# Optimization experiments

Hardware: AMD Instinct MI355X
Metric: run time of the kernel (lower is better)

Reference implementation:

```python
import jax, jax.numpy as jnp
import numpy as np

# Assumed sub-module definitions (NODETracker repo, sources not provided):
#   MLP(in,out)   = Linear -> LayerNorm -> LeakyReLU(0.1)
#   MLPODEF(dim,hidden,n_layers=2) = Linear(dim->h) -> tanh -> [Linear(h->h) -> tanh]*(n_layers-1) -> Linear(h->dim)
#   ode_solver_factory(None) -> fixed-step RK4, here 4 steps over t in [0,1]

LEAKY = 0.1
N_ODE_STEPS = 4
LATENT_DIM = 512
OBS_DIM = 256
HID_DIM = 1024
STATE = 2 * LATENT_DIM  # 1024
TIME_LEN = 128
BATCH = 512


def mlp_block(x, W, b, g, beta):
    h = x @ W + b
    mu = h.mean(-1, keepdims=True)
    var = ((h - mu) ** 2).mean(-1, keepdims=True)
    h = (h - mu) * jax.lax.rsqrt(var + 1e-5) * g + beta
    return jnp.where(h >= 0, h, LEAKY * h)


def odef(z, p):
    W0, b0, W1, b1, W2, b2 = p
    h = jnp.tanh(z @ W0 + b0)
    h = jnp.tanh(h @ W1 + b1)
    return h @ W2 + b2


def rk4_solve(z, p):
    dt = 1.0 / N_ODE_STEPS
    def step(z, _):
        k1 = odef(z, p)
        k2 = odef(z + 0.5 * dt * k1, p)
        k3 = odef(z + 0.5 * dt * k2, p)
        k4 = odef(z + dt * k3, p)
        return z + (dt / 6.0) * (k1 + 2 * k2 + 2 * k3 + k4), None
    z, _ = jax.lax.scan(step, z, None, length=N_ODE_STEPS)
    return z


def gru_step(x, h, W_ih, W_hh, b_ih, b_hh):
    gi = x @ W_ih.T + b_ih
    gh = h @ W_hh.T + b_hh
    i_r, i_z, i_n = jnp.split(gi, 3, axis=-1)
    h_r, h_z, h_n = jnp.split(gh, 3, axis=-1)
    r = jax.nn.sigmoid(i_r + h_r)
    zg = jax.nn.sigmoid(i_z + h_z)
    n = jnp.tanh(i_n + r * h_n)
    return (1.0 - zg) * n + zg * h


def setup_inputs() -> dict:
    key = jax.random.key(0)
    ks = jax.random.split(key, 16)
    def lin(k, fi, fo):
        return jax.random.normal(k, (fi, fo), jnp.float32) / np.sqrt(fi)
    return {
        'xs': jax.random.normal(ks[0], (TIME_LEN, BATCH, OBS_DIM), jnp.float32),
        'obs_W': lin(ks[1], OBS_DIM, HID_DIM), 'obs_b': jnp.zeros((HID_DIM,), jnp.float32),
        'obs_g': jnp.ones((HID_DIM,), jnp.float32), 'obs_beta': jnp.zeros((HID_DIM,), jnp.float32),
        'lat_W': lin(ks[2], HID_DIM, STATE), 'lat_b': jnp.zeros((STATE,), jnp.float32),
        'lat_g': jnp.ones((STATE,), jnp.float32), 'lat_beta': jnp.zeros((STATE,), jnp.float32),
        'ode_W0': lin(ks[3], STATE, HID_DIM), 'ode_b0': jnp.zeros((HID_DIM,), jnp.float32),
        'ode_W1': lin(ks[4], HID_DIM, HID_DIM), 'ode_b1': jnp.zeros((HID_DIM,), jnp.float32),
        'ode_W2': lin(ks[5], HID_DIM, STATE), 'ode_b2': jnp.zeros((STATE,), jnp.float32),
        'gru_Wih': jax.random.normal(ks[6], (3 * STATE, STATE), jnp.float32) / np.sqrt(STATE),
        'gru_Whh': jax.random.normal(ks[7], (3 * STATE, STATE), jnp.float32) / np.sqrt(STATE),
        'gru_bih': jnp.zeros((3 * STATE,), jnp.float32),
        'gru_bhh': jnp.zeros((3 * STATE,), jnp.float32),
    }


def reference(xs, obs_W, obs_b, obs_g, obs_beta, lat_W, lat_b, lat_g, lat_beta,
              ode_W0, ode_b0, ode_W1, ode_b1, ode_W2, ode_b2,
              gru_Wih, gru_Whh, gru_bih, gru_bhh):
    hs = mlp_block(xs, obs_W, obs_b, obs_g, obs_beta)          # [T,B,hid]
    zs = mlp_block(hs, lat_W, lat_b, lat_g, lat_beta)          # [T,B,2*latent]
    ode_p = (ode_W0, ode_b0, ode_W1, ode_b1, ode_W2, ode_b2)
    batch = xs.shape[1]
    h0 = jnp.zeros((batch, STATE), xs.dtype)

    def step(h, z_t):
        z = rk4_solve(z_t, ode_p)                               # NODE solve from t=0 to 1
        h_new = gru_step(z, h, gru_Wih, gru_Whh, gru_bih, gru_bhh)
        return h_new, None

    z0, _ = jax.lax.scan(step, h0, zs)                          # [B,2*latent]
    return z0[:, :LATENT_DIM], z0[:, LATENT_DIM:]
```

## Files before the change

### kernel.cpp

```cpp
#include <hip/hip_runtime.h>
#include <hip/hip_bf16.h>
#include <hip/hip_cooperative_groups.h>

namespace cg = cooperative_groups;

typedef __bf16 bf16_t;
typedef __bf16 bf16x8 __attribute__((ext_vector_type(8)));
typedef float f32x4 __attribute__((ext_vector_type(4)));

#define TLEN 128
#define BATCHN 512
#define OBS 256
#define HID 1024
#define STATEDIM 1024
#define ROWS (TLEN * BATCHN)
#define RKDT 0.25f

enum { EPI_F32 = 0, EPI_GI, EPI_TANH, EPI_Z0, EPI_Z0U, EPI_KW, EPI_KG, EPI_K4 };

__device__ __forceinline__ void gload_lds16(const bf16_t* g, bf16_t* l) {
  __builtin_amdgcn_global_load_lds(
      (const __attribute__((address_space(1))) void*)g,
      (__attribute__((address_space(3))) void*)l, 16, 0, 0);
}

__device__ __forceinline__ bf16_t f2bf(float x) { return (bf16_t)x; }

__device__ __forceinline__ float fast_tanh(float x) {
  const float e = __expf(2.f * x);
  return 1.f - 2.f / (e + 1.f);
}
__device__ __forceinline__ float fast_sigmoid(float x) {
  return 1.f / (1.f + __expf(-x));
}

#define MF(a_, b_, c_) __builtin_amdgcn_mfma_f32_16x16x32_bf16(a_, b_, c_, 0, 0, 0)

template<int EPI>
__global__ __launch_bounds__(256)
void gemm_bt(const bf16_t* __restrict__ A, const bf16_t* __restrict__ Wt,
             const float* __restrict__ bias, int M, int N, int K,
             float* outF, bf16_t* __restrict__ outB,
             float* Z, float* Z0,
             bf16_t* S2,
             const bf16_t* __restrict__ kb1, const bf16_t* __restrict__ kb2,
             const bf16_t* __restrict__ kb3,
             float kgc, int last)
{
  __shared__ __align__(16) bf16_t As[2][128 * 32];
  __shared__ __align__(16) bf16_t Bs[2][128 * 32];
  const int tid = threadIdx.x;
  const int lane = tid & 63;
  const int wave = tid >> 6;
  const int nbn = N >> 7;

  int bid = blockIdx.x;
  {
    const int nwg = gridDim.x;
    const int q = nwg >> 3, r = nwg & 7;
    const int xcd = bid & 7, lid = bid >> 3;
    bid = (xcd < r ? xcd * (q + 1) : r * (q + 1) + (xcd - r) * q) + lid;
  }
  const int bm = bid / nbn;
  const int bn = bid % nbn;
  const int m0 = bm << 7, n0 = bn << 7;
  const int wr = wave >> 1, wc = wave & 1;
  const int srow = tid >> 2;
  const int scol = (tid & 3) << 3;

  f32x4 acc[4][4] = {};
  const int nk = K >> 5;
  int cur = 0;

  {
    const bf16_t* ga = A  + (size_t)(m0 + srow) * K + scol;
    const bf16_t* gb = Wt + (size_t)(n0 + srow) * K + scol;
    bf16_t* la = &As[0][tid * 8];
    bf16_t* lb = &Bs[0][tid * 8];
    gload_lds16(ga, la);
    gload_lds16(ga + (size_t)64 * K, la + 2048);
    gload_lds16(gb, lb);
    gload_lds16(gb + (size_t)64 * K, lb + 2048);
  }

  for (int ks = 0; ks < nk; ++ks) {
    __syncthreads();
    if (ks + 1 < nk) {
      const bf16_t* ga = A  + (size_t)(m0 + srow) * K + (ks + 1) * 32 + scol;
      const bf16_t* gb = Wt + (size_t)(n0 + srow) * K + (ks + 1) * 32 + scol;
      bf16_t* la = &As[cur ^ 1][tid * 8];
      bf16_t* lb = &Bs[cur ^ 1][tid * 8];
      gload_lds16(ga, la);
      gload_lds16(ga + (size_t)64 * K, la + 2048);
      gload_lds16(gb, lb);
      gload_lds16(gb + (size_t)64 * K, lb + 2048);
    }
    const int kb = (lane >> 4) << 3;
    const int rr = lane & 15;
    bf16x8 af[4], bfr[4];
#pragma unroll
    for (int i = 0; i < 4; ++i) {
      af[i]  = *(const bf16x8*)&As[cur][(wr * 64 + i * 16 + rr) * 32 + kb];
      bfr[i] = *(const bf16x8*)&Bs[cur][(wc * 64 + i * 16 + rr) * 32 + kb];
    }
#pragma unroll
    for (int i = 0; i < 4; ++i)
#pragma unroll
      for (int j = 0; j < 4; ++j)
        acc[i][j] = MF(af[i], bfr[j], acc[i][j]);
    cur ^= 1;
  }

  const int cb = n0 + wc * 64 + (lane & 15);
  const int rb = m0 + wr * 64 + ((lane >> 4) << 2);
#pragma unroll
  for (int j = 0; j < 4; ++j) {
    const int c = cb + j * 16;
    float bv = 0.f;
    if constexpr (EPI != EPI_F32 && EPI != EPI_KG && EPI != EPI_Z0U) bv = bias[c];
#pragma unroll
    for (int i = 0; i < 4; ++i) {
      const int r0 = rb + i * 16;
#pragma unroll
      for (int r = 0; r < 4; ++r) {
        const size_t idx = (size_t)(r0 + r) * N + c;
        const float v = acc[i][j][r];
        if constexpr (EPI == EPI_F32) {
          outF[idx] = v;
        } else if constexpr (EPI == EPI_GI) {
          outF[idx] = v + bv;
        } else if constexpr (EPI == EPI_TANH) {
          outB[idx] = f2bf(fast_tanh(v + bv));
        } else if constexpr (EPI == EPI_Z0) {
          const float tz = v + bv;
          outF[idx] = tz;
          outB[idx] = f2bf(fast_tanh(tz));
        } else if constexpr (EPI == EPI_Z0U) {
          const float tz = Z0[idx] + v;
          Z0[idx] = tz;
          outB[idx] = f2bf(fast_tanh(tz));
        } else if constexpr (EPI == EPI_KW) {
          outB[idx] = f2bf(v + bv);
        } else if constexpr (EPI == EPI_KG) {
          outB[idx] = f2bf(fast_tanh(Z0[idx] + kgc * v));
        } else {
          const float k4 = v + bv;
          const float k1 = (float)kb1[idx];
          const float k2 = (float)kb2[idx];
          const float k3 = (float)kb3[idx];
          const float dz = (RKDT / 6.f) * (k1 + 2.f * k2 + 2.f * k3 + k4);
          const float zn = Z[idx] + dz;
          Z[idx] = zn;
          if (last) {
            const size_t si = (size_t)(r0 + r) * 2048 + c;
            const bf16_t hi = f2bf(zn);
            S2[si] = hi;
            S2[si + 1024] = f2bf(zn - (float)hi);
          } else {
            S2[idx] = f2bf(dz);
          }
        }
      }
    }
  }
}

__global__ __launch_bounds__(512)
void gru_persistent(const float* __restrict__ gi,
                    const bf16_t* __restrict__ Whh,
                    const float* __restrict__ bhh,
                    float* __restrict__ Hf,
                    bf16_t* __restrict__ hb,
                    unsigned int* __restrict__ ctr,
                    float* __restrict__ outp,
                    int TS, int t0)
{
  __shared__ __align__(16) bf16_t Bs[48 * 1032];
  const int tid  = threadIdx.x;
  const int lane = tid & 63;
  const int w    = tid >> 6;
  const int rg   = blockIdx.x >> 6;
  const int jg   = blockIdx.x & 63;
  const int r0   = rg << 7;
  const int j0   = jg << 4;

  for (int it = tid; it < 48 * 128; it += 512) {
    const int rr = it >> 7;
    const int co = (it & 127) << 3;
    const int g = rr >> 4, c = rr & 15;
    *(bf16x8*)&Bs[rr * 1032 + co] =
        *(const bf16x8*)&Whh[(size_t)(g * 1024 + j0 + c) * 1024 + co];
  }

  const int myj = j0 + (lane & 15);
  const float bh_r = bhh[myj], bh_z = bhh[1024 + myj], bh_n = bhh[2048 + myj];
  const int rbase = r0 + w * 16 + ((lane >> 4) << 2);

  float h[4];
#pragma unroll
  for (int q = 0; q < 4; ++q) h[q] = Hf[(size_t)(rbase + q) * 1024 + myj];

  float gpre[12];
  auto load_gi = [&](int lt) {
    const float* gir = gi + (size_t)lt * 512 * 3072;
#pragma unroll
    for (int q = 0; q < 4; ++q) {
      const size_t rr = (size_t)(rbase + q);
      gpre[q * 3 + 0] = gir[rr * 3072 + myj];
      gpre[q * 3 + 1] = gir[rr * 3072 + 1024 + myj];
      gpre[q * 3 + 2] = gir[rr * 3072 + 2048 + myj];
    }
  };
  load_gi(0);

  __syncthreads();

  const int arow = r0 + w * 16 + (lane & 15);
  const int akoff = (lane >> 4) << 3;

  for (int s = 0; s < TS; ++s) {
    const int t = t0 + s;
    const bf16_t* ap = hb + (size_t)(t & 1) * 512 * 2048 +
                       (size_t)arow * 2048 + akoff;
    f32x4 a0 = {}, a1 = {}, a2 = {};
    const bf16_t* bp0 = &Bs[(0  + (lane & 15)) * 1032 + akoff];
    const bf16_t* bp1 = &Bs[(16 + (lane & 15)) * 1032 + akoff];
    const bf16_t* bp2 = &Bs[(32 + (lane & 15)) * 1032 + akoff];
#pragma unroll 8
    for (int kc = 0; kc < 64; ++kc) {
      const bf16x8 af = *(const bf16x8*)(ap + kc * 32);
      const int kl = (kc * 32) & 1023;
      a0 = MF(af, *(const bf16x8*)(bp0 + kl), a0);
      a1 = MF(af, *(const bf16x8*)(bp1 + kl), a1);
      a2 = MF(af, *(const bf16x8*)(bp2 + kl), a2);
    }
    bf16_t* hbw = hb + (size_t)((t + 1) & 1) * 512 * 2048;
#pragma unroll
    for (int q = 0; q < 4; ++q) {
      const size_t rr = (size_t)(rbase + q);
      const float rg_ = fast_sigmoid(gpre[q * 3 + 0] + a0[q] + bh_r);
      const float zg  = fast_sigmoid(gpre[q * 3 + 1] + a1[q] + bh_z);
      const float n   = fast_tanh(gpre[q * 3 + 2] + rg_ * (a2[q] + bh_n));
      h[q] = (1.f - zg) * n + zg * h[q];
      union { __bf16 b; unsigned short u; } uh, ul;
      uh.b = f2bf(h[q]);
      ul.b = f2bf(h[q] - (float)uh.b);
      const unsigned ph = (unsigned)__shfl_xor((int)uh.u, 1) & 0xFFFFu;
      const unsigned pl = (unsigned)__shfl_xor((int)ul.u, 1) & 0xFFFFu;
      if (!(lane & 1)) {
        const unsigned hiw = (unsigned)uh.u | (ph << 16);
        const unsigned low = (unsigned)ul.u | (pl << 16);
        __hip_atomic_store((unsigned*)(hbw + rr * 2048 + myj), hiw,
                           __ATOMIC_RELAXED, __HIP_MEMORY_SCOPE_AGENT);
        __hip_atomic_store((unsigned*)(hbw + rr * 2048 + 1024 + myj), low,
                           __ATOMIC_RELAXED, __HIP_MEMORY_SCOPE_AGENT);
      }
    }
    if (s + 1 < TS) load_gi(s + 1);

    __syncthreads();
    if (tid == 0) {
      __hip_atomic_fetch_add(ctr, 1u, __ATOMIC_RELAXED, __HIP_MEMORY_SCOPE_AGENT);
      const unsigned tgt = 256u * (unsigned)(s + 1);
      while (__hip_atomic_load(ctr, __ATOMIC_ACQUIRE, __HIP_MEMORY_SCOPE_AGENT) < tgt)
        __builtin_amdgcn_s_sleep(1);
    }
    __syncthreads();
  }

#pragma unroll
  for (int q = 0; q < 4; ++q) {
    const int r = rbase + q;
    Hf[(size_t)r * 1024 + myj] = h[q];
    if (myj < 512) outp[(size_t)r * 512 + myj] = h[q];
    else           outp[262144 + (size_t)r * 512 + (myj - 512)] = h[q];
  }
}

__global__ void gru_reset(unsigned int* ctr) {
  if (threadIdx.x == 0)
    __hip_atomic_store(ctr, 0u, __ATOMIC_RELAXED, __HIP_MEMORY_SCOPE_AGENT);
}

template<bool SPLIT>
__global__ __launch_bounds__(256)
void ln_leaky(const float* __restrict__ pre, const float* __restrict__ b,
              const float* __restrict__ g, const float* __restrict__ bet,
              bf16_t* __restrict__ outB, float* __restrict__ zf)
{
  const int row = blockIdx.x;
  const int tid = threadIdx.x;
  const float* p = pre + (size_t)row * 1024;
  float v[4];
  float s = 0.f, s2 = 0.f;
#pragma unroll
  for (int i = 0; i < 4; ++i) {
    const int c = tid + i * 256;
    v[i] = p[c] + b[c];
    s += v[i]; s2 += v[i] * v[i];
  }
#pragma unroll
  for (int o = 32; o; o >>= 1) { s += __shfl_down(s, o); s2 += __shfl_down(s2, o); }
  __shared__ float rs[4], rs2[4];
  if ((tid & 63) == 0) { rs[tid >> 6] = s; rs2[tid >> 6] = s2; }
  __syncthreads();
  s = rs[0] + rs[1] + rs[2] + rs[3];
  s2 = rs2[0] + rs2[1] + rs2[2] + rs2[3];
  const float mu = s * (1.f / 1024.f);
  const float var = s2 * (1.f / 1024.f) - mu * mu;
  const float rstd = rsqrtf(var + 1e-5f);
#pragma unroll
  for (int i = 0; i < 4; ++i) {
    const int c = tid + i * 256;
    float h = (v[i] - mu) * rstd * g[c] + bet[c];
    h = h >= 0.f ? h : 0.1f * h;
    if constexpr (SPLIT) {
      const bf16_t hi = f2bf(h);
      outB[(size_t)row * 2048 + c] = hi;
      outB[(size_t)row * 2048 + 1024 + c] = f2bf(h - (float)hi);
      zf[(size_t)row * 1024 + c] = h;
    } else {
      outB[(size_t)row * 1024 + c] = f2bf(h);
    }
  }
}

__global__ __launch_bounds__(256)
void transpose_bf16(const float* __restrict__ in, bf16_t* __restrict__ out, int R, int C)
{
  __shared__ float t[32][33];
  const int c0 = blockIdx.x * 32, r0 = blockIdx.y * 32;
  const int tx = threadIdx.x & 31, ty = threadIdx.x >> 5;
#pragma unroll
  for (int i = 0; i < 32; i += 8)
    t[ty + i][tx] = in[(size_t)(r0 + ty + i) * C + c0 + tx];
  __syncthreads();
#pragma unroll
  for (int i = 0; i < 32; i += 8)
    out[(size_t)(c0 + ty + i) * R + r0 + tx] = f2bf(t[tx][ty + i]);
}

__global__ __launch_bounds__(256)
void f2b_kernel(const float* __restrict__ in, bf16_t* __restrict__ out, int n)
{
  const int i = blockIdx.x * 256 + threadIdx.x;
  if (i < n) out[i] = f2bf(in[i]);
}

__global__ __launch_bounds__(256)
void dup2_kernel(const bf16_t* __restrict__ in, bf16_t* __restrict__ out, int N, int K)
{
  const int idx = blockIdx.x * 256 + threadIdx.x;
  if (idx >= N * 2 * K) return;
  const int n = idx / (2 * K);
  const int kk = idx - n * 2 * K;
  const int k = kk < K ? kk : kk - K;
  out[idx] = in[(size_t)n * K + k];
}

__global__ void sentinel_kernel(float* out, float code) {
  if (threadIdx.x == 0 && blockIdx.x == 0) out[0] = code;
}

extern "C" void kernel_launch(void* const* d_in, const int* in_sizes, int n_in,
                              void* d_out, int out_size, void* d_ws, size_t ws_size,
                              hipStream_t stream)
{
  const float* xs    = (const float*)d_in[0];
  const float* obs_W = (const float*)d_in[1];
  const float* obs_b = (const float*)d_in[2];
  const float* obs_g = (const float*)d_in[3];
  const float* obs_be= (const float*)d_in[4];
  const float* lat_W = (const float*)d_in[5];
  const float* lat_b = (const float*)d_in[6];
  const float* lat_g = (const float*)d_in[7];
  const float* lat_be= (const float*)d_in[8];
  const float* W0    = (const float*)d_in[9];
  const float* b0    = (const float*)d_in[10];
  const float* W1    = (const float*)d_in[11];
  const float* b1    = (const float*)d_in[12];
  const float* W2    = (const float*)d_in[13];
  const float* b2    = (const float*)d_in[14];
  const float* Wih   = (const float*)d_in[15];
  const float* Whh   = (const float*)d_in[16];
  const float* bih   = (const float*)d_in[17];
  const float* bhh   = (const float*)d_in[18];

  char* ws = (char*)d_ws;
  size_t off = 0;
  auto alloc = [&](size_t bytes) { char* p = ws + off; off += bytes; return p; };

  bf16_t* OBSWT = (bf16_t*)alloc((size_t)HID * OBS * 2);
  bf16_t* LATWT = (bf16_t*)alloc((size_t)STATEDIM * HID * 2);
  bf16_t* W0T   = (bf16_t*)alloc((size_t)HID * STATEDIM * 2);
  bf16_t* W0T2  = (bf16_t*)alloc((size_t)HID * 2048 * 2);
  bf16_t* W1T   = (bf16_t*)alloc((size_t)HID * HID * 2);
  bf16_t* W2T   = (bf16_t*)alloc((size_t)STATEDIM * HID * 2);
  bf16_t* WIH2  = (bf16_t*)alloc((size_t)3072 * 2048 * 2);
  bf16_t* WHHB  = (bf16_t*)alloc((size_t)3072 * 1024 * 2);
  float*  Hf    = (float*)alloc((size_t)512 * 1024 * 4);
  bf16_t* HB2   = (bf16_t*)alloc((size_t)2 * 512 * 2048 * 2);
  bf16_t* WIHB  = (bf16_t*)alloc((size_t)3072 * 1024 * 2);
  bf16_t* XSB   = (bf16_t*)alloc((size_t)ROWS * OBS * 2);
  unsigned int* CTR = (unsigned int*)alloc(128);
  const size_t staticEnd = off;

  int nc = -1;
  const int ncs[8] = {1, 2, 4, 8, 16, 32, 64, 128};
  for (int i = 0; i < 8; ++i) {
    const size_t R = (size_t)ROWS / ncs[i];
    if (staticEnd + R * 22528 <= ws_size) { nc = ncs[i]; break; }
  }
  if (nc < 0) {
    sentinel_kernel<<<1, 1, 0, stream>>>((float*)d_out,
                                         -(1000000.0f + (float)(ws_size >> 20)));
    return;
  }
  const int R = ROWS / nc;
  char* arena = ws + staticEnd;
  float*  A1f  = (float*)(arena);
  bf16_t* KB1  = (bf16_t*)(arena);
  bf16_t* KB2  = (bf16_t*)(arena + (size_t)R * 2048);
  float*  Zf   = (float*)(arena + (size_t)R * 4096);
  float*  Z0f  = (float*)(arena + (size_t)R * 8192);
  bf16_t* H1b  = (bf16_t*)(arena + (size_t)R * 12288);
  bf16_t* H2b  = (bf16_t*)(arena + (size_t)R * 14336);
  bf16_t* KB3  = (bf16_t*)(arena + (size_t)R * 16384);
  bf16_t* S2b  = (bf16_t*)(arena + (size_t)R * 18432);
  bf16_t* DZb  = S2b;
  float*  GIf  = (float*)(arena);

  auto gemm = [&](int epi, const bf16_t* A, const bf16_t* Wt, const float* bias,
                  int M, int N, int K, float* oF, bf16_t* oB,
                  float kgc = 0.f, int last = 0) {
    dim3 g((M / 128) * (N / 128)), b(256);
    switch (epi) {
      case EPI_F32:  gemm_bt<EPI_F32><<<g, b, 0, stream>>>(A, Wt, bias, M, N, K, oF, oB, Zf, Z0f, S2b, KB1, KB2, KB3, kgc, last); break;
      case EPI_GI:   gemm_bt<EPI_GI><<<g, b, 0, stream>>>(A, Wt, bias, M, N, K, oF, oB, Zf, Z0f, S2b, KB1, KB2, KB3, kgc, last); break;
      case EPI_TANH: gemm_bt<EPI_TANH><<<g, b, 0, stream>>>(A, Wt, bias, M, N, K, oF, oB, Zf, Z0f, S2b, KB1, KB2, KB3, kgc, last); break;
      case EPI_Z0:   gemm_bt<EPI_Z0><<<g, b, 0, stream>>>(A, Wt, bias, M, N, K, oF, oB, Zf, Z0f, S2b, KB1, KB2, KB3, kgc, last); break;
      case EPI_Z0U:  gemm_bt<EPI_Z0U><<<g, b, 0, stream>>>(A, Wt, bias, M, N, K, oF, oB, Zf, Z0f, S2b, KB1, KB2, KB3, kgc, last); break;
      case EPI_KW:   gemm_bt<EPI_KW><<<g, b, 0, stream>>>(A, Wt, bias, M, N, K, oF, oB, Zf, Z0f, S2b, KB1, KB2, KB3, kgc, last); break;
      case EPI_KG:   gemm_bt<EPI_KG><<<g, b, 0, stream>>>(A, Wt, bias, M, N, K, oF, oB, Zf, Z0f, S2b, KB1, KB2, KB3, kgc, last); break;
      case EPI_K4:   gemm_bt<EPI_K4><<<g, b, 0, stream>>>(A, Wt, bias, M, N, K, oF, oB, Zf, Z0f, S2b, KB1, KB2, KB3, kgc, last); break;
    }
  };

  transpose_bf16<<<dim3(HID / 32, OBS / 32), 256, 0, stream>>>(obs_W, OBSWT, OBS, HID);
  transpose_bf16<<<dim3(STATEDIM / 32, HID / 32), 256, 0, stream>>>(lat_W, LATWT, HID, STATEDIM);
  transpose_bf16<<<dim3(HID / 32, STATEDIM / 32), 256, 0, stream>>>(W0, W0T, STATEDIM, HID);
  dup2_kernel<<<(HID * 2048) / 256, 256, 0, stream>>>(W0T, W0T2, HID, 1024);
  transpose_bf16<<<dim3(HID / 32, HID / 32), 256, 0, stream>>>(W1, W1T, HID, HID);
  transpose_bf16<<<dim3(STATEDIM / 32, HID / 32), 256, 0, stream>>>(W2, W2T, HID, STATEDIM);
  f2b_kernel<<<(3072 * 1024) / 256, 256, 0, stream>>>(Wih, WIHB, 3072 * 1024);
  dup2_kernel<<<(3072 * 2048) / 256, 256, 0, stream>>>(WIHB, WIH2, 3072, 1024);
  f2b_kernel<<<(3072 * 1024) / 256, 256, 0, stream>>>(Whh, WHHB, 3072 * 1024);
  f2b_kernel<<<(ROWS * OBS) / 256, 256, 0, stream>>>(xs, XSB, ROWS * OBS);

  hipMemsetAsync(Hf, 0, (size_t)512 * 1024 * 4, stream);
  hipMemsetAsync(HB2, 0, (size_t)2 * 512 * 2048 * 2, stream);
  const int TS = R / BATCHN;

  for (int c = 0; c < nc; ++c) {
    gemm(EPI_F32, XSB + (size_t)c * R * OBS, OBSWT, nullptr, R, HID, OBS, A1f, nullptr);
    ln_leaky<false><<<R, 256, 0, stream>>>(A1f, obs_b, obs_g, obs_be, H1b, nullptr);
    gemm(EPI_F32, H1b, LATWT, nullptr, R, STATEDIM, HID, A1f, nullptr);
    ln_leaky<true><<<R, 256, 0, stream>>>(A1f, lat_b, lat_g, lat_be, S2b, Zf);

    for (int step = 0; step < 4; ++step) {
      if (step == 0) gemm(EPI_Z0, S2b, W0T2, b0, R, HID, 2048, Z0f, H1b);
      else           gemm(EPI_Z0U, DZb, W0T, nullptr, R, HID, 1024, nullptr, H1b);
      gemm(EPI_TANH, H1b, W1T, b1, R, HID, HID, nullptr, H2b);
      gemm(EPI_KW, H2b, W2T, b2, R, STATEDIM, HID, nullptr, KB1);
      gemm(EPI_KG, KB1, W0T, nullptr, R, HID, STATEDIM, nullptr, H1b, 0.5f * RKDT);
      gemm(EPI_TANH, H1b, W1T, b1, R, HID, HID, nullptr, H2b);
      gemm(EPI_KW, H2b, W2T, b2, R, STATEDIM, HID, nullptr, KB2);
      gemm(EPI_KG, KB2, W0T, nullptr, R, HID, STATEDIM, nullptr, H1b, 0.5f * RKDT);
      gemm(EPI_TANH, H1b, W1T, b1, R, HID, HID, nullptr, H2b);
      gemm(EPI_KW, H2b, W2T, b2, R, STATEDIM, HID, nullptr, KB3);
      gemm(EPI_KG, KB3, W0T, nullptr, R, HID, STATEDIM, nullptr, H1b, RKDT);
      gemm(EPI_TANH, H1b, W1T, b1, R, HID, HID, nullptr, H2b);
      gemm(EPI_K4, H2b, W2T, b2, R, STATEDIM, HID, nullptr, nullptr, 0.f,
           (step == 3) ? 1 : 0);
    }

    gemm(EPI_GI, S2b, WIH2, bih, R, 3072, 2048, GIf, nullptr);

    gru_reset<<<1, 64, 0, stream>>>(CTR);
    {
      const float* giArg = GIf;
      const bf16_t* whhArg = WHHB;
      const float* bhhArg = bhh;
      float* hfArg = Hf;
      bf16_t* hbArg = HB2;
      unsigned int* ctrArg = CTR;
      float* outArg = (float*)d_out;
      int tsArg = TS;
      int t0Arg = c * TS;
      void* args[] = { (void*)&giArg, (void*)&whhArg, (void*)&bhhArg,
                       (void*)&hfArg, (void*)&hbArg, (void*)&ctrArg,
                       (void*)&outArg, (void*)&tsArg, (void*)&t0Arg };
      hipLaunchCooperativeKernel((const void*)gru_persistent,
                                 dim3(256), dim3(512), args, 0, stream);
    }
  }
}
```

Measured before the change: 18.83 ms.

## Fuse RK4 ODE GEMM chain into one cooperative persistent kernel with grid barriers

Runs the 52 per-chunk ODE GEMM stages inside a single cooperatively launched persistent kernel. Blocks loop over 128x128 tiles in an XCD-aware order and synchronise between stages with an atomic-counter grid barrier. Epilogue stores become agent-scope relaxed atomic stores, packed as bf16 pairs through lane shuffles, so writes are visible across the grid. This is meant to remove per-launch overhead and inter-kernel gaps, at the cost of barrier spin time, occupancy capped at two blocks per CU, and the extra shuffle work on the store path. The original multi-launch path stays as a fallback if the cooperative launch fails.

```diff
diff --git a/kernel.cpp b/kernel.cpp
--- a/kernel.cpp
+++ b/kernel.cpp
@@ -75,12 +75,10 @@
   {
     const bf16_t* ga = A  + (size_t)(m0 + srow) * K + scol;
     const bf16_t* gb = Wt + (size_t)(n0 + srow) * K + scol;
-    bf16_t* la = &As[0][tid * 8];
-    bf16_t* lb = &Bs[0][tid * 8];
-    gload_lds16(ga, la);
-    gload_lds16(ga + (size_t)64 * K, la + 2048);
-    gload_lds16(gb, lb);
-    gload_lds16(gb + (size_t)64 * K, lb + 2048);
+    gload_lds16(ga, &As[0][tid * 8]);
+    gload_lds16(ga + (size_t)64 * K, &As[0][tid * 8] + 2048);
+    gload_lds16(gb, &Bs[0][tid * 8]);
+    gload_lds16(gb + (size_t)64 * K, &Bs[0][tid * 8] + 2048);
   }
 
   for (int ks = 0; ks < nk; ++ks) {
@@ -88,12 +86,10 @@
     if (ks + 1 < nk) {
       const bf16_t* ga = A  + (size_t)(m0 + srow) * K + (ks + 1) * 32 + scol;
       const bf16_t* gb = Wt + (size_t)(n0 + srow) * K + (ks + 1) * 32 + scol;
-      bf16_t* la = &As[cur ^ 1][tid * 8];
-      bf16_t* lb = &Bs[cur ^ 1][tid * 8];
-      gload_lds16(ga, la);
-      gload_lds16(ga + (size_t)64 * K, la + 2048);
-      gload_lds16(gb, lb);
-      gload_lds16(gb + (size_t)64 * K, lb + 2048);
+      gload_lds16(ga, &As[cur ^ 1][tid * 8]);
+      gload_lds16(ga + (size_t)64 * K, &As[cur ^ 1][tid * 8] + 2048);
+      gload_lds16(gb, &Bs[cur ^ 1][tid * 8]);
+      gload_lds16(gb + (size_t)64 * K, &Bs[cur ^ 1][tid * 8] + 2048);
     }
     const int kb = (lane >> 4) << 3;
     const int rr = lane & 15;
@@ -165,6 +161,197 @@
   }
 }
 
+__device__ __forceinline__ void sc1_f32(float* p, float v) {
+  __hip_atomic_store(p, v, __ATOMIC_RELAXED, __HIP_MEMORY_SCOPE_AGENT);
+}
+__device__ __forceinline__ void sc1_bf16pair(bf16_t* base, size_t idx, float val, int lane) {
+  union { __bf16 b; unsigned short u; } t; t.b = f2bf(val);
+  const unsigned other = (unsigned)__shfl_xor((int)t.u, 1) & 0xFFFFu;
+  if (!(lane & 1)) {
+    const unsigned wv = (unsigned)t.u | (other << 16);
+    __hip_atomic_store((unsigned*)(base + idx), wv,
+                       __ATOMIC_RELAXED, __HIP_MEMORY_SCOPE_AGENT);
+  }
+}
+
+__device__ __forceinline__ void grid_bar(unsigned* ctr, int bar) {
+  __syncthreads();
+  if (threadIdx.x == 0) {
+    __hip_atomic_fetch_add(ctr, 1u, __ATOMIC_RELAXED, __HIP_MEMORY_SCOPE_AGENT);
+    const unsigned tgt = (unsigned)gridDim.x * (unsigned)bar;
+    while (__hip_atomic_load(ctr, __ATOMIC_ACQUIRE, __HIP_MEMORY_SCOPE_AGENT) < tgt)
+      __builtin_amdgcn_s_sleep(1);
+  }
+  __syncthreads();
+}
+
+template<int EPI>
+__device__ void ode_stage(const bf16_t* __restrict__ A, const bf16_t* __restrict__ Wt,
+                          const float* __restrict__ bias, int R, int K,
+                          float kgc, int last,
+                          float* Zf, float* Z0f, bf16_t* outB, bf16_t* S2,
+                          const bf16_t* __restrict__ kb1, const bf16_t* __restrict__ kb2,
+                          const bf16_t* __restrict__ kb3,
+                          bf16_t* as_base, bf16_t* bs_base)
+{
+  const int tid = threadIdx.x;
+  const int lane = tid & 63;
+  const int wave = tid >> 6;
+  const int wr = wave >> 1, wc = wave & 1;
+  const int srow = tid >> 2;
+  const int scol = (tid & 3) << 3;
+  const int nk = K >> 5;
+  const int ntiles = (R >> 7) << 3;
+  const int cpx = ntiles >> 3;
+
+  for (int tt = blockIdx.x; tt < ntiles; tt += gridDim.x) {
+    const int ts = (tt & 7) * cpx + (tt >> 3);
+    const int m0 = (ts >> 3) << 7, n0 = (ts & 7) << 7;
+    f32x4 acc[4][4] = {};
+    int cur = 0;
+    {
+      const bf16_t* ga = A  + (size_t)(m0 + srow) * K + scol;
+      const bf16_t* gb = Wt + (size_t)(n0 + srow) * K + scol;
+      gload_lds16(ga, as_base + tid * 8);
+      gload_lds16(ga + (size_t)64 * K, as_base + tid * 8 + 2048);
+      gload_lds16(gb, bs_base + tid * 8);
+      gload_lds16(gb + (size_t)64 * K, bs_base + tid * 8 + 2048);
+    }
+    for (int ks = 0; ks < nk; ++ks) {
+      __syncthreads();
+      if (ks + 1 < nk) {
+        const bf16_t* ga = A  + (size_t)(m0 + srow) * K + (ks + 1) * 32 + scol;
+        const bf16_t* gb = Wt + (size_t)(n0 + srow) * K + (ks + 1) * 32 + scol;
+        gload_lds16(ga, as_base + (cur ^ 1) * 4096 + tid * 8);
+        gload_lds16(ga + (size_t)64 * K, as_base + (cur ^ 1) * 4096 + tid * 8 + 2048);
+        gload_lds16(gb, bs_base + (cur ^ 1) * 4096 + tid * 8);
+        gload_lds16(gb + (size_t)64 * K, bs_base + (cur ^ 1) * 4096 + tid * 8 + 2048);
+      }
+      const int kb = (lane >> 4) << 3;
+      const int rr = lane & 15;
+      bf16x8 af[4], bfr[4];
+#pragma unroll
+      for (int i = 0; i < 4; ++i) {
+        af[i]  = *(const bf16x8*)(as_base + cur * 4096 + (wr * 64 + i * 16 + rr) * 32 + kb);
+        bfr[i] = *(const bf16x8*)(bs_base + cur * 4096 + (wc * 64 + i * 16 + rr) * 32 + kb);
+      }
+#pragma unroll
+      for (int i = 0; i < 4; ++i)
+#pragma unroll
+        for (int j = 0; j < 4; ++j)
+          acc[i][j] = MF(af[i], bfr[j], acc[i][j]);
+      cur ^= 1;
+    }
+
+    const int cb = n0 + wc * 64 + (lane & 15);
+    const int rb = m0 + wr * 64 + ((lane >> 4) << 2);
+#pragma unroll
+    for (int j = 0; j < 4; ++j) {
+      const int c = cb + j * 16;
+      float bv = 0.f;
+      if constexpr (EPI == EPI_Z0 || EPI == EPI_TANH || EPI == EPI_KW || EPI == EPI_K4)
+        bv = bias[c];
+#pragma unroll
+      for (int i = 0; i < 4; ++i) {
+        const int r0 = rb + i * 16;
+#pragma unroll
+        for (int r = 0; r < 4; ++r) {
+          const size_t idx = (size_t)(r0 + r) * 1024 + c;
+          const float v = acc[i][j][r];
+          if constexpr (EPI == EPI_Z0) {
+            const float tz = v + bv;
+            sc1_f32(&Z0f[idx], tz);
+            sc1_bf16pair(outB, idx, fast_tanh(tz), lane);
+          } else if constexpr (EPI == EPI_Z0U) {
+            const float tz = Z0f[idx] + v;
+            sc1_f32(&Z0f[idx], tz);
+            sc1_bf16pair(outB, idx, fast_tanh(tz), lane);
+          } else if constexpr (EPI == EPI_TANH) {
+            sc1_bf16pair(outB, idx, fast_tanh(v + bv), lane);
+          } else if constexpr (EPI == EPI_KW) {
+            sc1_bf16pair(outB, idx, v + bv, lane);
+          } else if constexpr (EPI == EPI_KG) {
+            sc1_bf16pair(outB, idx, fast_tanh(Z0f[idx] + kgc * v), lane);
+          } else {
+            const float k4 = v + bv;
+            const float k1 = (float)kb1[idx];
+            const float k2 = (float)kb2[idx];
+            const float k3 = (float)kb3[idx];
+            const float dz = (RKDT / 6.f) * (k1 + 2.f * k2 + 2.f * k3 + k4);
+            const float zn = Zf[idx] + dz;
+            sc1_f32(&Zf[idx], zn);
+            if (last) {
+              const size_t si = (size_t)(r0 + r) * 2048 + c;
+              const float hi = (float)f2bf(zn);
+              sc1_bf16pair(S2, si, zn, lane);
+              sc1_bf16pair(S2, si + 1024, zn - hi, lane);
+            } else {
+              sc1_bf16pair(S2, idx, dz, lane);
+            }
+          }
+        }
+      }
+    }
+  }
+}
+
+__global__ __launch_bounds__(256, 2)
+void ode_persistent(const bf16_t* __restrict__ W0T2, const bf16_t* __restrict__ W0T,
+                    const bf16_t* __restrict__ W1T, const bf16_t* __restrict__ W2T,
+                    const float* __restrict__ b0, const float* __restrict__ b1,
+                    const float* __restrict__ b2,
+                    float* Zf, float* Z0f, bf16_t* H1b, bf16_t* H2b,
+                    bf16_t* KB1, bf16_t* KB2, bf16_t* KB3, bf16_t* S2b,
+                    unsigned* ctr, int R)
+{
+  __shared__ __align__(16) bf16_t As[2 * 4096];
+  __shared__ __align__(16) bf16_t Bs[2 * 4096];
+  int bar = 0;
+#pragma unroll 1
+  for (int step = 0; step < 4; ++step) {
+    if (step == 0)
+      ode_stage<EPI_Z0>(S2b, W0T2, b0, R, 2048, 0.f, 0, Zf, Z0f, H1b, S2b,
+                        nullptr, nullptr, nullptr, As, Bs);
+    else
+      ode_stage<EPI_Z0U>(S2b, W0T, nullptr, R, 1024, 0.f, 0, Zf, Z0f, H1b, S2b,
+                         nullptr, nullptr, nullptr, As, Bs);
+    grid_bar(ctr, ++bar);
+    ode_stage<EPI_TANH>(H1b, W1T, b1, R, 1024, 0.f, 0, Zf, Z0f, H2b, S2b,
+                        nullptr, nullptr, nullptr, As, Bs);
+    grid_bar(ctr, ++bar);
+    ode_stage<EPI_KW>(H2b, W2T, b2, R, 1024, 0.f, 0, Zf, Z0f, KB1, S2b,
+                      nullptr, nullptr, nullptr, As, Bs);
+    grid_bar(ctr, ++bar);
+    ode_stage<EPI_KG>(KB1, W0T, nullptr, R, 1024, 0.5f * RKDT, 0, Zf, Z0f, H1b, S2b,
+                      nullptr, nullptr, nullptr, As, Bs);
+    grid_bar(ctr, ++bar);
+    ode_stage<EPI_TANH>(H1b, W1T, b1, R, 1024, 0.f, 0, Zf, Z0f, H2b, S2b,
+                        nullptr, nullptr, nullptr, As, Bs);
+    grid_bar(ctr, ++bar);
+    ode_stage<EPI_KW>(H2b, W2T, b2, R, 1024, 0.f, 0, Zf, Z0f, KB2, S2b,
+                      nullptr, nullptr, nullptr, As, Bs);
+    grid_bar(ctr, ++bar);
+    ode_stage<EPI_KG>(KB2, W0T, nullptr, R, 1024, 0.5f * RKDT, 0, Zf, Z0f, H1b, S2b,
+                      nullptr, nullptr, nullptr, As, Bs);
+    grid_bar(ctr, ++bar);
+    ode_stage<EPI_TANH>(H1b, W1T, b1, R, 1024, 0.f, 0, Zf, Z0f, H2b, S2b,
+                        nullptr, nullptr, nullptr, As, Bs);
+    grid_bar(ctr, ++bar);
+    ode_stage<EPI_KW>(H2b, W2T, b2, R, 1024, 0.f, 0, Zf, Z0f, KB3, S2b,
+                      nullptr, nullptr, nullptr, As, Bs);
+    grid_bar(ctr, ++bar);
+    ode_stage<EPI_KG>(KB3, W0T, nullptr, R, 1024, RKDT, 0, Zf, Z0f, H1b, S2b,
+                      nullptr, nullptr, nullptr, As, Bs);
+    grid_bar(ctr, ++bar);
+    ode_stage<EPI_TANH>(H1b, W1T, b1, R, 1024, 0.f, 0, Zf, Z0f, H2b, S2b,
+                        nullptr, nullptr, nullptr, As, Bs);
+    grid_bar(ctr, ++bar);
+    ode_stage<EPI_K4>(H2b, W2T, b2, R, 1024, 0.f, (step == 3) ? 1 : 0,
+                      Zf, Z0f, nullptr, S2b, KB1, KB2, KB3, As, Bs);
+    grid_bar(ctr, ++bar);
+  }
+}
+
 __global__ __launch_bounds__(512)
 void gru_persistent(const float* __restrict__ gi,
                     const bf16_t* __restrict__ Whh,
@@ -277,7 +464,7 @@
   }
 }
 
-__global__ void gru_reset(unsigned int* ctr) {
+__global__ void ctr_reset(unsigned int* ctr) {
   if (threadIdx.x == 0)
     __hip_atomic_store(ctr, 0u, __ATOMIC_RELAXED, __HIP_MEMORY_SCOPE_AGENT);
 }
@@ -402,7 +589,8 @@
   bf16_t* HB2   = (bf16_t*)alloc((size_t)2 * 512 * 2048 * 2);
   bf16_t* WIHB  = (bf16_t*)alloc((size_t)3072 * 1024 * 2);
   bf16_t* XSB   = (bf16_t*)alloc((size_t)ROWS * OBS * 2);
-  unsigned int* CTR = (unsigned int*)alloc(128);
+  unsigned int* GCTR = (unsigned int*)alloc(128);
+  unsigned int* OCTR = (unsigned int*)alloc(128);
   const size_t staticEnd = off;
 
   int nc = -1;
@@ -461,39 +649,64 @@
   hipMemsetAsync(HB2, 0, (size_t)2 * 512 * 2048 * 2, stream);
   const int TS = R / BATCHN;
 
+  int occ = 0;
+  (void)hipOccupancyMaxActiveBlocksPerMultiprocessor(
+      &occ, (const void*)ode_persistent, 256, 0);
+  const int odeBlocks = (occ >= 2) ? 512 : (occ == 1 ? 256 : 0);
+
   for (int c = 0; c < nc; ++c) {
     gemm(EPI_F32, XSB + (size_t)c * R * OBS, OBSWT, nullptr, R, HID, OBS, A1f, nullptr);
     ln_leaky<false><<<R, 256, 0, stream>>>(A1f, obs_b, obs_g, obs_be, H1b, nullptr);
     gemm(EPI_F32, H1b, LATWT, nullptr, R, STATEDIM, HID, A1f, nullptr);
     ln_leaky<true><<<R, 256, 0, stream>>>(A1f, lat_b, lat_g, lat_be, S2b, Zf);
 
-    for (int step = 0; step < 4; ++step) {
-      if (step == 0) gemm(EPI_Z0, S2b, W0T2, b0, R, HID, 2048, Z0f, H1b);
-      else           gemm(EPI_Z0U, DZb, W0T, nullptr, R, HID, 1024, nullptr, H1b);
-      gemm(EPI_TANH, H1b, W1T, b1, R, HID, HID, nullptr, H2b);
-      gemm(EPI_KW, H2b, W2T, b2, R, STATEDIM, HID, nullptr, KB1);
-      gemm(EPI_KG, KB1, W0T, nullptr, R, HID, STATEDIM, nullptr, H1b, 0.5f * RKDT);
-      gemm(EPI_TANH, H1b, W1T, b1, R, HID, HID, nullptr, H2b);
-      gemm(EPI_KW, H2b, W2T, b2, R, STATEDIM, HID, nullptr, KB2);
-      gemm(EPI_KG, KB2, W0T, nullptr, R, HID, STATEDIM, nullptr, H1b, 0.5f * RKDT);
-      gemm(EPI_TANH, H1b, W1T, b1, R, HID, HID, nullptr, H2b);
-      gemm(EPI_KW, H2b, W2T, b2, R, STATEDIM, HID, nullptr, KB3);
-      gemm(EPI_KG, KB3, W0T, nullptr, R, HID, STATEDIM, nullptr, H1b, RKDT);
-      gemm(EPI_TANH, H1b, W1T, b1, R, HID, HID, nullptr, H2b);
-      gemm(EPI_K4, H2b, W2T, b2, R, STATEDIM, HID, nullptr, nullptr, 0.f,
-           (step == 3) ? 1 : 0);
+    bool persisted = false;
+    if (odeBlocks > 0) {
+      ctr_reset<<<1, 64, 0, stream>>>(OCTR);
+      const bf16_t* a0_ = W0T2; const bf16_t* a1_ = W0T;
+      const bf16_t* a2_ = W1T;  const bf16_t* a3_ = W2T;
+      const float* a4_ = b0; const float* a5_ = b1; const float* a6_ = b2;
+      float* a7_ = Zf; float* a8_ = Z0f;
+      bf16_t* a9_ = H1b; bf16_t* a10_ = H2b;
+      bf16_t* a11_ = KB1; bf16_t* a12_ = KB2; bf16_t* a13_ = KB3;
+      bf16_t* a14_ = S2b;
+      unsigned int* a15_ = OCTR; int a16_ = R;
+      void* args[] = { &a0_, &a1_, &a2_, &a3_, &a4_, &a5_, &a6_, &a7_, &a8_,
+                       &a9_, &a10_, &a11_, &a12_, &a13_, &a14_, &a15_, &a16_ };
+      hipError_t e = hipLaunchCooperativeKernel((const void*)ode_persistent,
+                                                dim3(odeBlocks), dim3(256),
+                                                args, 0, stream);
+      persisted = (e == hipSuccess);
+    }
+    if (!persisted) {
+      for (int step = 0; step < 4; ++step) {
+        if (step == 0) gemm(EPI_Z0, S2b, W0T2, b0, R, HID, 2048, Z0f, H1b);
+        else           gemm(EPI_Z0U, DZb, W0T, nullptr, R, HID, 1024, nullptr, H1b);
+        gemm(EPI_TANH, H1b, W1T, b1, R, HID, HID, nullptr, H2b);
+        gemm(EPI_KW, H2b, W2T, b2, R, STATEDIM, HID, nullptr, KB1);
+        gemm(EPI_KG, KB1, W0T, nullptr, R, HID, STATEDIM, nullptr, H1b, 0.5f * RKDT);
+        gemm(EPI_TANH, H1b, W1T, b1, R, HID, HID, nullptr, H2b);
+        gemm(EPI_KW, H2b, W2T, b2, R, STATEDIM, HID, nullptr, KB2);
+        gemm(EPI_KG, KB2, W0T, nullptr, R, HID, STATEDIM, nullptr, H1b, 0.5f * RKDT);
+        gemm(EPI_TANH, H1b, W1T, b1, R, HID, HID, nullptr, H2b);
+        gemm(EPI_KW, H2b, W2T, b2, R, STATEDIM, HID, nullptr, KB3);
+        gemm(EPI_KG, KB3, W0T, nullptr, R, HID, STATEDIM, nullptr, H1b, RKDT);
+        gemm(EPI_TANH, H1b, W1T, b1, R, HID, HID, nullptr, H2b);
+        gemm(EPI_K4, H2b, W2T, b2, R, STATEDIM, HID, nullptr, nullptr, 0.f,
+             (step == 3) ? 1 : 0);
+      }
     }
 
     gemm(EPI_GI, S2b, WIH2, bih, R, 3072, 2048, GIf, nullptr);
 
-    gru_reset<<<1, 64, 0, stream>>>(CTR);
+    ctr_reset<<<1, 64, 0, stream>>>(GCTR);
     {
       const float* giArg = GIf;
       const bf16_t* whhArg = WHHB;
       const float* bhhArg = bhh;
       float* hfArg = Hf;
       bf16_t* hbArg = HB2;
-      unsigned int* ctrArg = CTR;
+      unsigned int* ctrArg = GCTR;
       float* outArg = (float*)d_out;
       int tsArg = TS;
       int t0Arg = c * TS;
```

After: 31.96 ms. 1.7x slower.

## Fold W0 into W2 to fuse RK stage GEMMs and accumulate stages in fp32

Applied to the files above, without the earlier changes.

Precomputes the combined weight W0·W2 and bias, and concatenates it with W2 so each RK stage runs one N=2048 GEMM. That GEMM produces both k and the next stage's pre-activation directly, instead of a W2 GEMM followed by a W0 GEMM on k. Stage contributions are accumulated in fp32 KACC/GACC buffers, and Z0 is updated in the fourth-stage epilogue, which removes the per-step Z0 update GEMM and the bf16 k buffers. This reduces launches and intermediate memory traffic, at the cost of wider epilogue branches and slightly different numerics from the pre-multiplied weights.

```diff
diff --git a/kernel.cpp b/kernel.cpp
--- a/kernel.cpp
+++ b/kernel.cpp
@@ -16,7 +16,7 @@
 #define ROWS (TLEN * BATCHN)
 #define RKDT 0.25f
 
-enum { EPI_F32 = 0, EPI_GI, EPI_TANH, EPI_Z0, EPI_Z0U, EPI_KW, EPI_KG, EPI_K4 };
+enum { EPI_F32 = 0, EPI_GI, EPI_TANH, EPI_B16, EPI_Z0, EPI_F1, EPI_F23, EPI_F4, EPI_K4L };
 
 __device__ __forceinline__ void gload_lds16(const bf16_t* g, bf16_t* l) {
   __builtin_amdgcn_global_load_lds(
@@ -41,10 +41,8 @@
 void gemm_bt(const bf16_t* __restrict__ A, const bf16_t* __restrict__ Wt,
              const float* __restrict__ bias, int M, int N, int K,
              float* outF, bf16_t* __restrict__ outB,
-             float* Z, float* Z0,
-             bf16_t* S2,
-             const bf16_t* __restrict__ kb1, const bf16_t* __restrict__ kb2,
-             const bf16_t* __restrict__ kb3,
+             float* Z, float* Z0, bf16_t* S2,
+             float* KACC, float* GACC,
              float kgc, int last)
 {
   __shared__ __align__(16) bf16_t As[2][128 * 32];
@@ -117,7 +115,7 @@
   for (int j = 0; j < 4; ++j) {
     const int c = cb + j * 16;
     float bv = 0.f;
-    if constexpr (EPI != EPI_F32 && EPI != EPI_KG && EPI != EPI_Z0U) bv = bias[c];
+    if constexpr (EPI != EPI_F32 && EPI != EPI_B16) bv = bias[c];
 #pragma unroll
     for (int i = 0; i < 4; ++i) {
       const int r0 = rb + i * 16;
@@ -131,34 +129,45 @@
           outF[idx] = v + bv;
         } else if constexpr (EPI == EPI_TANH) {
           outB[idx] = f2bf(fast_tanh(v + bv));
+        } else if constexpr (EPI == EPI_B16) {
+          outB[idx] = f2bf(v);
         } else if constexpr (EPI == EPI_Z0) {
           const float tz = v + bv;
           outF[idx] = tz;
           outB[idx] = f2bf(fast_tanh(tz));
-        } else if constexpr (EPI == EPI_Z0U) {
-          const float tz = Z0[idx] + v;
-          Z0[idx] = tz;
-          outB[idx] = f2bf(fast_tanh(tz));
-        } else if constexpr (EPI == EPI_KW) {
-          outB[idx] = f2bf(v + bv);
-        } else if constexpr (EPI == EPI_KG) {
-          outB[idx] = f2bf(fast_tanh(Z0[idx] + kgc * v));
+        } else if constexpr (EPI == EPI_F1 || EPI == EPI_F23) {
+          if (c < 1024) {
+            const size_t ix = (size_t)(r0 + r) * 1024 + c;
+            const float kv = v + bv;
+            if constexpr (EPI == EPI_F1) KACC[ix] = (RKDT / 6.f) * kv;
+            else                         KACC[ix] += (RKDT / 3.f) * kv;
+          } else {
+            const size_t ix = (size_t)(r0 + r) * 1024 + (c - 1024);
+            const float Gv = v + bv;
+            outB[ix] = f2bf(fast_tanh(Z0[ix] + kgc * Gv));
+            if constexpr (EPI == EPI_F1) GACC[ix] = (RKDT / 6.f) * Gv;
+            else                         GACC[ix] += (RKDT / 3.f) * Gv;
+          }
+        } else if constexpr (EPI == EPI_F4) {
+          if (c < 1024) {
+            const size_t ix = (size_t)(r0 + r) * 1024 + c;
+            const float kv = v + bv;
+            Z[ix] = Z[ix] + KACC[ix] + (RKDT / 6.f) * kv;
+          } else {
+            const size_t ix = (size_t)(r0 + r) * 1024 + (c - 1024);
+            const float Gv = v + bv;
+            const float z0n = Z0[ix] + GACC[ix] + (RKDT / 6.f) * Gv;
+            Z0[ix] = z0n;
+            outB[ix] = f2bf(fast_tanh(z0n));
+          }
         } else {
-          const float k4 = v + bv;
-          const float k1 = (float)kb1[idx];
-          const float k2 = (float)kb2[idx];
-          const float k3 = (float)kb3[idx];
-          const float dz = (RKDT / 6.f) * (k1 + 2.f * k2 + 2.f * k3 + k4);
-          const float zn = Z[idx] + dz;
+          const float kv = v + bv;
+          const float zn = Z[idx] + KACC[idx] + (RKDT / 6.f) * kv;
           Z[idx] = zn;
-          if (last) {
-            const size_t si = (size_t)(r0 + r) * 2048 + c;
-            const bf16_t hi = f2bf(zn);
-            S2[si] = hi;
-            S2[si + 1024] = f2bf(zn - (float)hi);
-          } else {
-            S2[idx] = f2bf(dz);
-          }
+          const size_t si = (size_t)(r0 + r) * 2048 + c;
+          const bf16_t hi = f2bf(zn);
+          S2[si] = hi;
+          S2[si + 1024] = f2bf(zn - (float)hi);
         }
       }
     }
@@ -358,6 +367,18 @@
   out[idx] = in[(size_t)n * K + k];
 }
 
+__global__ __launch_bounds__(256)
+void biaskg_kernel(const float* __restrict__ b2, const float* __restrict__ W0,
+                   float* __restrict__ biasKG)
+{
+  const int n = blockIdx.x * 256 + threadIdx.x;
+  if (n >= 1024) return;
+  biasKG[n] = b2[n];
+  float s = 0.f;
+  for (int ss = 0; ss < 1024; ++ss) s += b2[ss] * W0[(size_t)ss * 1024 + n];
+  biasKG[1024 + n] = s;
+}
+
 __global__ void sentinel_kernel(float* out, float code) {
   if (threadIdx.x == 0 && blockIdx.x == 0) out[0] = code;
 }
@@ -395,13 +416,15 @@
   bf16_t* W0T   = (bf16_t*)alloc((size_t)HID * STATEDIM * 2);
   bf16_t* W0T2  = (bf16_t*)alloc((size_t)HID * 2048 * 2);
   bf16_t* W1T   = (bf16_t*)alloc((size_t)HID * HID * 2);
-  bf16_t* W2T   = (bf16_t*)alloc((size_t)STATEDIM * HID * 2);
+  bf16_t* WKG   = (bf16_t*)alloc((size_t)2048 * 1024 * 2);
+  bf16_t* W2B   = (bf16_t*)alloc((size_t)HID * STATEDIM * 2);
   bf16_t* WIH2  = (bf16_t*)alloc((size_t)3072 * 2048 * 2);
   bf16_t* WHHB  = (bf16_t*)alloc((size_t)3072 * 1024 * 2);
   float*  Hf    = (float*)alloc((size_t)512 * 1024 * 4);
   bf16_t* HB2   = (bf16_t*)alloc((size_t)2 * 512 * 2048 * 2);
   bf16_t* WIHB  = (bf16_t*)alloc((size_t)3072 * 1024 * 2);
   bf16_t* XSB   = (bf16_t*)alloc((size_t)ROWS * OBS * 2);
+  float*  biasKG= (float*)alloc((size_t)2048 * 4);
   unsigned int* CTR = (unsigned int*)alloc(128);
   const size_t staticEnd = off;
 
@@ -409,7 +432,7 @@
   const int ncs[8] = {1, 2, 4, 8, 16, 32, 64, 128};
   for (int i = 0; i < 8; ++i) {
     const size_t R = (size_t)ROWS / ncs[i];
-    if (staticEnd + R * 22528 <= ws_size) { nc = ncs[i]; break; }
+    if (staticEnd + R * 20480 <= ws_size) { nc = ncs[i]; break; }
   }
   if (nc < 0) {
     sentinel_kernel<<<1, 1, 0, stream>>>((float*)d_out,
@@ -419,15 +442,13 @@
   const int R = ROWS / nc;
   char* arena = ws + staticEnd;
   float*  A1f  = (float*)(arena);
-  bf16_t* KB1  = (bf16_t*)(arena);
-  bf16_t* KB2  = (bf16_t*)(arena + (size_t)R * 2048);
+  float*  KACC = (float*)(arena);
   float*  Zf   = (float*)(arena + (size_t)R * 4096);
   float*  Z0f  = (float*)(arena + (size_t)R * 8192);
   bf16_t* H1b  = (bf16_t*)(arena + (size_t)R * 12288);
   bf16_t* H2b  = (bf16_t*)(arena + (size_t)R * 14336);
-  bf16_t* KB3  = (bf16_t*)(arena + (size_t)R * 16384);
-  bf16_t* S2b  = (bf16_t*)(arena + (size_t)R * 18432);
-  bf16_t* DZb  = S2b;
+  bf16_t* S2b  = (bf16_t*)(arena + (size_t)R * 16384);
+  float*  GACC = (float*)(arena + (size_t)R * 16384);
   float*  GIf  = (float*)(arena);
 
   auto gemm = [&](int epi, const bf16_t* A, const bf16_t* Wt, const float* bias,
@@ -435,14 +456,15 @@
                   float kgc = 0.f, int last = 0) {
     dim3 g((M / 128) * (N / 128)), b(256);
     switch (epi) {
-      case EPI_F32:  gemm_bt<EPI_F32><<<g, b, 0, stream>>>(A, Wt, bias, M, N, K, oF, oB, Zf, Z0f, S2b, KB1, KB2, KB3, kgc, last); break;
-      case EPI_GI:   gemm_bt<EPI_GI><<<g, b, 0, stream>>>(A, Wt, bias, M, N, K, oF, oB, Zf, Z0f, S2b, KB1, KB2, KB3, kgc, last); break;
-      case EPI_TANH: gemm_bt<EPI_TANH><<<g, b, 0, stream>>>(A, Wt, bias, M, N, K, oF, oB, Zf, Z0f, S2b, KB1, KB2, KB3, kgc, last); break;
-      case EPI_Z0:   gemm_bt<EPI_Z0><<<g, b, 0, stream>>>(A, Wt, bias, M, N, K, oF, oB, Zf, Z0f, S2b, KB1, KB2, KB3, kgc, last); break;
-      case EPI_Z0U:  gemm_bt<EPI_Z0U><<<g, b, 0, stream>>>(A, Wt, bias, M, N, K, oF, oB, Zf, Z0f, S2b, KB1, KB2, KB3, kgc, last); break;
-      case EPI_KW:   gemm_bt<EPI_KW><<<g, b, 0, stream>>>(A, Wt, bias, M, N, K, oF, oB, Zf, Z0f, S2b, KB1, KB2, KB3, kgc, last); break;
-      case EPI_KG:   gemm_bt<EPI_KG><<<g, b, 0, stream>>>(A, Wt, bias, M, N, K, oF, oB, Zf, Z0f, S2b, KB1, KB2, KB3, kgc, last); break;
-      case EPI_K4:   gemm_bt<EPI_K4><<<g, b, 0, stream>>>(A, Wt, bias, M, N, K, oF, oB, Zf, Z0f, S2b, KB1, KB2, KB3, kgc, last); break;
+      case EPI_F32:  gemm_bt<EPI_F32><<<g, b, 0, stream>>>(A, Wt, bias, M, N, K, oF, oB, Zf, Z0f, S2b, KACC, GACC, kgc, last); break;
+      case EPI_GI:   gemm_bt<EPI_GI><<<g, b, 0, stream>>>(A, Wt, bias, M, N, K, oF, oB, Zf, Z0f, S2b, KACC, GACC, kgc, last); break;
+      case EPI_TANH: gemm_bt<EPI_TANH><<<g, b, 0, stream>>>(A, Wt, bias, M, N, K, oF, oB, Zf, Z0f, S2b, KACC, GACC, kgc, last); break;
+      case EPI_B16:  gemm_bt<EPI_B16><<<g, b, 0, stream>>>(A, Wt, bias, M, N, K, oF, oB, Zf, Z0f, S2b, KACC, GACC, kgc, last); break;
+      case EPI_Z0:   gemm_bt<EPI_Z0><<<g, b, 0, stream>>>(A, Wt, bias, M, N, K, oF, oB, Zf, Z0f, S2b, KACC, GACC, kgc, last); break;
+      case EPI_F1:   gemm_bt<EPI_F1><<<g, b, 0, stream>>>(A, Wt, bias, M, N, K, oF, oB, Zf, Z0f, S2b, KACC, GACC, kgc, last); break;
+      case EPI_F23:  gemm_bt<EPI_F23><<<g, b, 0, stream>>>(A, Wt, bias, M, N, K, oF, oB, Zf, Z0f, S2b, KACC, GACC, kgc, last); break;
+      case EPI_F4:   gemm_bt<EPI_F4><<<g, b, 0, stream>>>(A, Wt, bias, M, N, K, oF, oB, Zf, Z0f, S2b, KACC, GACC, kgc, last); break;
+      case EPI_K4L:  gemm_bt<EPI_K4L><<<g, b, 0, stream>>>(A, Wt, bias, M, N, K, oF, oB, Zf, Z0f, S2b, KACC, GACC, kgc, last); break;
     }
   };
 
@@ -451,7 +473,10 @@
   transpose_bf16<<<dim3(HID / 32, STATEDIM / 32), 256, 0, stream>>>(W0, W0T, STATEDIM, HID);
   dup2_kernel<<<(HID * 2048) / 256, 256, 0, stream>>>(W0T, W0T2, HID, 1024);
   transpose_bf16<<<dim3(HID / 32, HID / 32), 256, 0, stream>>>(W1, W1T, HID, HID);
-  transpose_bf16<<<dim3(STATEDIM / 32, HID / 32), 256, 0, stream>>>(W2, W2T, HID, STATEDIM);
+  transpose_bf16<<<dim3(STATEDIM / 32, HID / 32), 256, 0, stream>>>(W2, WKG, HID, STATEDIM);
+  f2b_kernel<<<(HID * STATEDIM) / 256, 256, 0, stream>>>(W2, W2B, HID * STATEDIM);
+  gemm(EPI_B16, W0T, W2B, nullptr, 1024, 1024, 1024, nullptr, WKG + (size_t)1024 * 1024);
+  biaskg_kernel<<<4, 256, 0, stream>>>(b2, W0, biasKG);
   f2b_kernel<<<(3072 * 1024) / 256, 256, 0, stream>>>(Wih, WIHB, 3072 * 1024);
   dup2_kernel<<<(3072 * 2048) / 256, 256, 0, stream>>>(WIHB, WIH2, 3072, 1024);
   f2b_kernel<<<(3072 * 1024) / 256, 256, 0, stream>>>(Whh, WHHB, 3072 * 1024);
@@ -467,21 +492,20 @@
     gemm(EPI_F32, H1b, LATWT, nullptr, R, STATEDIM, HID, A1f, nullptr);
     ln_leaky<true><<<R, 256, 0, stream>>>(A1f, lat_b, lat_g, lat_be, S2b, Zf);
 
+    gemm(EPI_Z0, S2b, W0T2, b0, R, HID, 2048, Z0f, H1b);
+
     for (int step = 0; step < 4; ++step) {
-      if (step == 0) gemm(EPI_Z0, S2b, W0T2, b0, R, HID, 2048, Z0f, H1b);
-      else           gemm(EPI_Z0U, DZb, W0T, nullptr, R, HID, 1024, nullptr, H1b);
       gemm(EPI_TANH, H1b, W1T, b1, R, HID, HID, nullptr, H2b);
-      gemm(EPI_KW, H2b, W2T, b2, R, STATEDIM, HID, nullptr, KB1);
-      gemm(EPI_KG, KB1, W0T, nullptr, R, HID, STATEDIM, nullptr, H1b, 0.5f * RKDT);
+      gemm(EPI_F1, H2b, WKG, biasKG, R, 2048, HID, nullptr, H1b, 0.5f * RKDT);
       gemm(EPI_TANH, H1b, W1T, b1, R, HID, HID, nullptr, H2b);
-      gemm(EPI_KW, H2b, W2T, b2, R, STATEDIM, HID, nullptr, KB2);
-      gemm(EPI_KG, KB2, W0T, nullptr, R, HID, STATEDIM, nullptr, H1b, 0.5f * RKDT);
+      gemm(EPI_F23, H2b, WKG, biasKG, R, 2048, HID, nullptr, H1b, 0.5f * RKDT);
       gemm(EPI_TANH, H1b, W1T, b1, R, HID, HID, nullptr, H2b);
-      gemm(EPI_KW, H2b, W2T, b2, R, STATEDIM, HID, nullptr, KB3);
-      gemm(EPI_KG, KB3, W0T, nullptr, R, HID, STATEDIM, nullptr, H1b, RKDT);
+      gemm(EPI_F23, H2b, WKG, biasKG, R, 2048, HID, nullptr, H1b, RKDT);
       gemm(EPI_TANH, H1b, W1T, b1, R, HID, HID, nullptr, H2b);
-      gemm(EPI_K4, H2b, W2T, b2, R, STATEDIM, HID, nullptr, nullptr, 0.f,
-           (step == 3) ? 1 : 0);
+      if (step < 3)
+        gemm(EPI_F4, H2b, WKG, biasKG, R, 2048, HID, nullptr, H1b);
+      else
+        gemm(EPI_K4L, H2b, WKG, b2, R, STATEDIM, HID, nullptr, nullptr);
     }
 
     gemm(EPI_GI, S2b, WIH2, bih, R, 3072, 2048, GIf, nullptr);
```

Result: slower. 21.26 ms (+12.9%).
